# Kernel tuning notes

Hardware: AMD Instinct MI355X
Metric: run time of the kernel (lower is better)

Reference implementation:

```python
import jax, jax.numpy as jnp
import numpy as np

EMB = 1024
HEADS = 16
HEAD_DIM = EMB // HEADS
CTX = 2048
BATCH = 4
LN_EPS = 1e-5


def layer_norm(x, g, b):
    mu = jnp.mean(x, axis=-1, keepdims=True)
    var = jnp.mean(jnp.square(x - mu), axis=-1, keepdims=True)
    return (x - mu) * jax.lax.rsqrt(var + LN_EPS) * g + b


def setup_inputs() -> dict:
    key = jax.random.key(0)
    ks = jax.random.split(key, 12)
    s_in = 1.0 / np.sqrt(EMB)
    s_ff = 1.0 / np.sqrt(4 * EMB)
    return {
        "x": jax.random.normal(ks[0], (BATCH, CTX, EMB), jnp.float32),
        # per-head Q/K/V projections, no bias (matches Head linears)
        "wq": jax.random.normal(ks[1], (HEADS, EMB, HEAD_DIM), jnp.float32) * s_in,
        "wk": jax.random.normal(ks[2], (HEADS, EMB, HEAD_DIM), jnp.float32) * s_in,
        "wv": jax.random.normal(ks[3], (HEADS, EMB, HEAD_DIM), jnp.float32) * s_in,
        "w_proj": jax.random.normal(ks[4], (EMB, EMB), jnp.float32) * s_in,
        "b_proj": jnp.zeros((EMB,), jnp.float32),
        "w1": jax.random.normal(ks[5], (EMB, 4 * EMB), jnp.float32) * s_in,
        "b1": jnp.zeros((4 * EMB,), jnp.float32),
        "w2": jax.random.normal(ks[6], (4 * EMB, EMB), jnp.float32) * s_ff,
        "b2": jnp.zeros((EMB,), jnp.float32),
        "ln1_g": jnp.ones((EMB,), jnp.float32),
        "ln1_b": jnp.zeros((EMB,), jnp.float32),
        "ln2_g": jnp.ones((EMB,), jnp.float32),
        "ln2_b": jnp.zeros((EMB,), jnp.float32),
    }


def reference(x, wq, wk, wv, w_proj, b_proj, w1, b1, w2, b2, ln1_g, ln1_b, ln2_g, ln2_b):
    B, T, C = x.shape
    # --- attention branch (pre-LN) ---
    h = layer_norm(x, ln1_g, ln1_b)
    q = jnp.einsum('btc,hcd->bhtd', h, wq)
    k = jnp.einsum('btc,hcd->bhtd', h, wk)
    v = jnp.einsum('btc,hcd->bhtd', h, wv)
    scale = 1.0 / np.sqrt(HEAD_DIM)
    scores = jnp.einsum('bhtd,bhsd->bhts', q, k) * scale  # [B,H,T,T]
    causal = jnp.tril(jnp.ones((T, T), dtype=bool))
    scores = jnp.where(causal, scores, -jnp.inf)
    attn = jax.nn.softmax(scores, axis=-1)
    out = jnp.einsum('bhts,bhsd->bhtd', attn, v)
    out = out.transpose(0, 2, 1, 3).reshape(B, T, C)  # concat heads
    out = out @ w_proj.T + b_proj if False else jnp.einsum('btc,cd->btd', out, w_proj) + b_proj
    x = x + out
    # --- FFN branch (pre-LN) ---
    h2 = layer_norm(x, ln2_g, ln2_b)
    ff = jax.nn.relu(jnp.einsum('btc,cf->btf', h2, w1) + b1)
    ff = jnp.einsum('btf,fc->btc', ff, w2) + b2
    return x + ff
```

## Files before the change

kernel.cpp:

```cpp
#include <hip/hip_runtime.h>


#define DEVI __device__ __forceinline__

typedef float  f32x4  __attribute__((ext_vector_type(4)));
typedef float  f32x16 __attribute__((ext_vector_type(16)));
typedef __bf16 bf16x8 __attribute__((ext_vector_type(8)));
typedef short  s16x8  __attribute__((ext_vector_type(8)));
typedef unsigned int u32x4 __attribute__((ext_vector_type(4)));
typedef unsigned short u16;

DEVI u16 f2bf(float f) {
    return __builtin_bit_cast(u16, (__bf16)f);
}

DEVI float bf2f(u16 u) {
    unsigned v = (unsigned)u << 16;
    return __builtin_bit_cast(float, v);
}

DEVI unsigned pk2(float lo, float hi2) {
    return (unsigned)f2bf(lo) | ((unsigned)f2bf(hi2) << 16);
}

DEVI void gload_lds16(const void* g, void* l) {
    __builtin_amdgcn_global_load_lds(
        (__attribute__((address_space(1))) void*)(g),
        (__attribute__((address_space(3))) void*)(l), 16, 0, 0);
}

DEVI f32x4 mfma16(s16x8 a, s16x8 b, f32x4 c) {
    return __builtin_amdgcn_mfma_f32_16x16x32_bf16(
        __builtin_bit_cast(bf16x8, a), __builtin_bit_cast(bf16x8, b), c, 0, 0, 0);
}

DEVI f32x16 mfma32(s16x8 a, s16x8 b, f32x16 c) {
    return __builtin_amdgcn_mfma_f32_32x32x16_bf16(
        __builtin_bit_cast(bf16x8, a), __builtin_bit_cast(bf16x8, b), c, 0, 0, 0);
}

__global__ __launch_bounds__(256) void transpose_cvt(
    const float* __restrict__ src, u16* __restrict__ dst,
    int K, int N, long srcStride, long dstStride)
{
    __shared__ float t[64][65];
    src += (long)blockIdx.z * srcStride;
    dst += (long)blockIdx.z * dstStride;
    int k0 = blockIdx.x * 64, n0 = blockIdx.y * 64;
    int tx = threadIdx.x & 63, ty = threadIdx.x >> 6;
#pragma unroll
    for (int i = 0; i < 16; ++i) {
        int r = ty * 16 + i;
        t[r][tx] = src[(long)(k0 + r) * N + n0 + tx];
    }
    __syncthreads();
#pragma unroll
    for (int i = 0; i < 16; ++i) {
        int r = ty * 16 + i;
        dst[(long)(n0 + r) * K + k0 + tx] = f2bf(t[tx][r]);
    }
}

__global__ __launch_bounds__(256) void ln_bf16(
    const float* __restrict__ x, const float* __restrict__ g,
    const float* __restrict__ b, u16* __restrict__ out)
{
    int row = blockIdx.x, tid = threadIdx.x;
    const float4 v = ((const float4*)(x + (long)row * 1024))[tid];
    float s = v.x + v.y + v.z + v.w;
    float q = v.x * v.x + v.y * v.y + v.z * v.z + v.w * v.w;
#pragma unroll
    for (int m = 1; m < 64; m <<= 1) { s += __shfl_xor(s, m); q += __shfl_xor(q, m); }
    __shared__ float red[8];
    int lane = tid & 63, w = tid >> 6;
    if (lane == 0) { red[w] = s; red[w + 4] = q; }
    __syncthreads();
    s = red[0] + red[1] + red[2] + red[3];
    q = red[4] + red[5] + red[6] + red[7];
    float mu  = s * (1.0f / 1024.0f);
    float var = q * (1.0f / 1024.0f) - mu * mu;
    float rs  = rsqrtf(var + 1e-5f);
    float4 gv = ((const float4*)g)[tid];
    float4 bv = ((const float4*)b)[tid];
    ushort4 o;
    o.x = f2bf((v.x - mu) * rs * gv.x + bv.x);
    o.y = f2bf((v.y - mu) * rs * gv.y + bv.y);
    o.z = f2bf((v.z - mu) * rs * gv.z + bv.z);
    o.w = f2bf((v.w - mu) * rs * gv.w + bv.w);
    ((ushort4*)(out + (long)row * 1024))[tid] = o;
}

template <int EPI>
__global__ __launch_bounds__(512, 4) void gemm_big(
    const u16* __restrict__ A, const u16* __restrict__ Bt,
    int M, int N, int K,
    u16* __restrict__ outB, const float* __restrict__ bias,
    u16* __restrict__ qd, u16* __restrict__ kd, u16* __restrict__ vd)
{
    __shared__ alignas(16) u16 As[256 * 32];
    __shared__ alignas(16) u16 Bs[128 * 32];
    int tid = threadIdx.x;
    int lane = tid & 63, w = tid >> 6;
    int wm = w >> 1, wn = w & 1;
    int l15 = lane & 15, l4 = lane >> 4;
    long m0 = (long)blockIdx.x * 256, n0 = (long)blockIdx.y * 128;
    const u16* Ag = A + m0 * K;
    const u16* Bg = Bt + n0 * K;
    int srow_l = lane >> 2;
    int schunk = ((lane & 3) ^ (srow_l & 3)) * 8;
    int rchunk = (l4 ^ (l15 & 3)) * 8;

    f32x4 acc[4][4] = {};

    for (int kt = 0; kt < K; kt += 32) {
        gload_lds16(Ag + (long)(w * 32 + srow_l) * K + kt + schunk,
                    &As[(w * 32) * 32]);
        gload_lds16(Ag + (long)(w * 32 + 16 + srow_l) * K + kt + schunk,
                    &As[(w * 32 + 16) * 32]);
        gload_lds16(Bg + (long)(w * 16 + srow_l) * K + kt + schunk,
                    &Bs[(w * 16) * 32]);
        __syncthreads();
        s16x8 a[4], b[4];
#pragma unroll
        for (int m = 0; m < 4; ++m)
            a[m] = *(const s16x8*)&As[(wm * 64 + m * 16 + l15) * 32 + rchunk];
#pragma unroll
        for (int n = 0; n < 4; ++n)
            b[n] = *(const s16x8*)&Bs[(wn * 64 + n * 16 + l15) * 32 + rchunk];
#pragma unroll
        for (int m = 0; m < 4; ++m)
#pragma unroll
            for (int n = 0; n < 4; ++n)
                acc[m][n] = mfma16(a[m], b[n], acc[m][n]);
        __syncthreads();
    }

    long mbase = m0 + wm * 64;
    long nbase = n0 + wn * 64;
#pragma unroll
    for (int m = 0; m < 4; ++m)
#pragma unroll
        for (int n = 0; n < 4; ++n)
#pragma unroll
            for (int r = 0; r < 4; ++r) {
                long row = mbase + m * 16 + l4 * 4 + r;
                long col = nbase + n * 16 + l15;
                float val = acc[m][n][r];
                if constexpr (EPI == 0) {
                    int c = (int)col;
                    int which = c >> 10, hh = (c >> 6) & 15, dd = c & 63;
                    int bb = (int)(row >> 11), tt = (int)(row & 2047);
                    if (which == 2) {
                        vd[((long)(bb * 16 + hh) * 64 + dd) * 2048 + tt] = f2bf(val);
                    } else {
                        u16* dst = which == 0 ? qd : kd;
                        dst[((long)(bb * 16 + hh) * 2048 + tt) * 64 + dd] = f2bf(val);
                    }
                } else {
                    float t2 = val + bias[col];
                    outB[row * N + col] = f2bf(t2 > 0.f ? t2 : 0.f);
                }
            }
}

template <int EPI>
__global__ __launch_bounds__(256, 3) void gemm_bt(
    const u16* __restrict__ A, const u16* __restrict__ Bt,
    int M, int N, int K,
    float* __restrict__ outF, u16* __restrict__ outB,
    const float* __restrict__ bias, const float* __restrict__ resid,
    u16* __restrict__ qd, u16* __restrict__ kd, u16* __restrict__ vd)
{
    __shared__ alignas(16) u16 As[128 * 32];
    __shared__ alignas(16) u16 Bs[128 * 32];
    int tid = threadIdx.x;
    int lane = tid & 63, w = tid >> 6;
    int wm = w & 1, wn = w >> 1;
    int l15 = lane & 15, l4 = lane >> 4;
    long m0 = (long)blockIdx.x * 128, n0 = (long)blockIdx.y * 128;
    const u16* Ag = A + m0 * K;
    const u16* Bg = Bt + n0 * K;
    int scol = ((lane & 3) ^ ((lane >> 2) & 3)) * 8;
    int srow0 = (w * 2 + 0) * 16 + (lane >> 2);
    int srow1 = (w * 2 + 1) * 16 + (lane >> 2);
    int rchunk = (l4 ^ (l15 & 3)) * 8;

    f32x4 acc[4][4] = {};

    for (int kt = 0; kt < K; kt += 32) {
        gload_lds16(Ag + (long)srow0 * K + kt + scol, &As[(w * 2 + 0) * 512]);
        gload_lds16(Ag + (long)srow1 * K + kt + scol, &As[(w * 2 + 1) * 512]);
        gload_lds16(Bg + (long)srow0 * K + kt + scol, &Bs[(w * 2 + 0) * 512]);
        gload_lds16(Bg + (long)srow1 * K + kt + scol, &Bs[(w * 2 + 1) * 512]);
        __syncthreads();
        s16x8 a[4], b[4];
#pragma unroll
        for (int m = 0; m < 4; ++m)
            a[m] = *(const s16x8*)&As[(wm * 64 + m * 16 + l15) * 32 + rchunk];
#pragma unroll
        for (int n = 0; n < 4; ++n)
            b[n] = *(const s16x8*)&Bs[(wn * 64 + n * 16 + l15) * 32 + rchunk];
#pragma unroll
        for (int m = 0; m < 4; ++m)
#pragma unroll
            for (int n = 0; n < 4; ++n)
                acc[m][n] = mfma16(a[m], b[n], acc[m][n]);
        __syncthreads();
    }

    long mbase = m0 + wm * 64;
    long nbase = n0 + wn * 64;
#pragma unroll
    for (int m = 0; m < 4; ++m)
#pragma unroll
        for (int n = 0; n < 4; ++n)
#pragma unroll
            for (int r = 0; r < 4; ++r) {
                long row = mbase + m * 16 + l4 * 4 + r;
                long col = nbase + n * 16 + l15;
                float val = acc[m][n][r];
                if constexpr (EPI == 1) {
                    outF[row * N + col] = val + bias[col] + resid[row * N + col];
                }
            }
}

__global__ __launch_bounds__(256, 4) void attn_split(
    const u16* __restrict__ Q, const u16* __restrict__ K,
    const u16* __restrict__ Vt,
    u16* __restrict__ Op0, u16* __restrict__ Op1, float* __restrict__ ML)
{
    constexpr int PAD = 72;
    constexpr float SC2 = 0.125f * 1.44269504088896f;
    constexpr float THR = 11.5416f;
    __shared__ alignas(16) u16 Ks[2][64 * PAD];
    __shared__ alignas(16) u16 Vts[2][64 * PAD];
    __shared__ alignas(16) float xbuf[4][32];
    int tid = threadIdx.x, lane = tid & 63, w = tid >> 6;
    int l31 = lane & 31, hi = lane >> 5;
    bool h = (hi != 0);
    int p = blockIdx.x, hh = blockIdx.y, bb = blockIdx.z;
    const long hbase = ((long)(bb * 16 + hh)) * 2048 * 64;
    const long rb = ((long)(bb * 16 + hh)) * 2048;

    int srow[2], scol8[2];
#pragma unroll
    for (int i = 0; i < 2; ++i) {
        int c = tid + 256 * i;
        srow[i] = c >> 3;
        scol8[i] = (c & 7) * 8;
    }

#pragma unroll 1
    for (int ph = 0; ph < 2; ++ph) {
        int qt  = ph == 0 ? p : 15 - p;
        int kt0 = ph == 0 ? 0 : (qt + 1);
        int kt1 = qt + 1 + ph * (qt + 1);
        int ntl = kt1 - kt0;
        int q0w = qt * 128 + w * 32;
        int qv = q0w + l31;

        s16x8 bq[4];
#pragma unroll
        for (int c = 0; c < 4; ++c)
            bq[c] = *(const s16x8*)&Q[hbase + (long)(q0w + l31) * 64 + c * 16 + hi * 8];

        f32x16 o0 = {}, o1 = {};
        float mrow = -1e30f, lrow = 0.f;

        s16x8 kr[2], vr[2];
        {
            const u16* Kg = K + hbase + (long)kt0 * 64 * 64;
            const u16* Vg = Vt + hbase + (long)kt0 * 64;
#pragma unroll
            for (int i = 0; i < 2; ++i) {
                s16x8 k0 = *(const s16x8*)&Kg[srow[i] * 64 + scol8[i]];
                s16x8 v0 = *(const s16x8*)&Vg[(long)srow[i] * 2048 + scol8[i]];
                *(s16x8*)&Ks[0][srow[i] * PAD + scol8[i]]  = k0;
                *(s16x8*)&Vts[0][srow[i] * PAD + scol8[i]] = v0;
            }
            if (ntl > 1) {
                const u16* Kg1 = K + hbase + (long)(kt0 + 1) * 64 * 64;
                const u16* Vg1 = Vt + hbase + (long)(kt0 + 1) * 64;
#pragma unroll
                for (int i = 0; i < 2; ++i) {
                    kr[i] = *(const s16x8*)&Kg1[srow[i] * 64 + scol8[i]];
                    vr[i] = *(const s16x8*)&Vg1[(long)srow[i] * 2048 + scol8[i]];
                }
            }
        }
        __syncthreads();

#pragma unroll 1
        for (int j = 0; j < ntl; ++j) {
            int kt = kt0 + j;
            int cur = j & 1;
            if (j + 1 < ntl) {
#pragma unroll
                for (int i = 0; i < 2; ++i) {
                    *(s16x8*)&Ks[cur ^ 1][srow[i] * PAD + scol8[i]]  = kr[i];
                    *(s16x8*)&Vts[cur ^ 1][srow[i] * PAD + scol8[i]] = vr[i];
                }
            }
            if (j + 2 < ntl) {
                const u16* Kg = K + hbase + (long)(kt + 2) * 64 * 64;
                const u16* Vg = Vt + hbase + (long)(kt + 2) * 64;
#pragma unroll
                for (int i = 0; i < 2; ++i) {
                    kr[i] = *(const s16x8*)&Kg[srow[i] * 64 + scol8[i]];
                    vr[i] = *(const s16x8*)&Vg[(long)srow[i] * 2048 + scol8[i]];
                }
            }

#pragma unroll
            for (int k2 = 0; k2 < 2; ++k2) {
                int kbase = kt * 64 + k2 * 32;
                if (kbase <= q0w + 31) {
                    f32x16 s = {};
                    __builtin_amdgcn_s_setprio(1);
#pragma unroll
                    for (int c = 0; c < 4; ++c) {
                        s16x8 ak = *(const s16x8*)&Ks[cur][(k2 * 32 + l31) * PAD + c * 16 + hi * 8];
                        s = mfma32(ak, bq[c], s);
                    }
                    __builtin_amdgcn_s_setprio(0);

                    if (kbase + 31 > q0w) {
                        int d = qv - (kbase + 4 * hi);
#pragma unroll
                        for (int r = 0; r < 16; ++r) {
                            int pat = (r & 3) + 8 * (r >> 2);
                            if (pat > d) s[r] = -3.0e38f;
                        }
                    }

                    float t8[8], t4[4];
#pragma unroll
                    for (int r = 0; r < 8; ++r) t8[r] = fmaxf(s[r], s[r + 8]);
#pragma unroll
                    for (int r = 0; r < 4; ++r) t4[r] = fmaxf(t8[r], t8[r + 4]);
                    float pm = fmaxf(fmaxf(t4[0], t4[2]), fmaxf(t4[1], t4[3]));
                    pm *= SC2;
                    pm = fmaxf(pm, __shfl_xor(pm, 32));

                    int allok = __all(pm - mrow <= THR);
                    float ef = 1.f;
                    if (!allok) {
                        float mn = fmaxf(mrow, pm);
                        ef = exp2f(mrow - mn);
                        mrow = mn;
                    }
#pragma unroll
                    for (int r = 0; r < 16; ++r) s[r] = exp2f(fmaf(s[r], SC2, -mrow));
                    float a8[8], a4[4];
#pragma unroll
                    for (int r = 0; r < 8; ++r) a8[r] = s[r] + s[r + 8];
#pragma unroll
                    for (int r = 0; r < 4; ++r) a4[r] = a8[r] + a8[r + 4];
                    float rsum = (a4[0] + a4[1]) + (a4[2] + a4[3]);
                    rsum += __shfl_xor(rsum, 32);

                    if (!allok) {
                        lrow = lrow * ef + rsum;
                        xbuf[w][l31] = ef;
#pragma unroll
                        for (int rr = 0; rr < 4; ++rr) {
                            f32x4 efv = *(const f32x4*)&xbuf[w][rr * 8 + hi * 4];
#pragma unroll
                            for (int j2 = 0; j2 < 4; ++j2) {
                                o0[rr * 4 + j2] *= efv[j2];
                                o1[rr * 4 + j2] *= efv[j2];
                            }
                        }
                    } else {
                        lrow += rsum;
                    }

                    unsigned c0 = pk2(s[0],  s[1]),  c1 = pk2(s[2],  s[3]);
                    unsigned c2 = pk2(s[4],  s[5]),  c3 = pk2(s[6],  s[7]);
                    unsigned c4 = pk2(s[8],  s[9]),  c5 = pk2(s[10], s[11]);
                    unsigned c6 = pk2(s[12], s[13]), c7 = pk2(s[14], s[15]);
                    unsigned x0 = __shfl_xor((int)c0, 32), x1 = __shfl_xor((int)c1, 32);
                    unsigned x2 = __shfl_xor((int)c2, 32), x3 = __shfl_xor((int)c3, 32);
                    unsigned x4 = __shfl_xor((int)c4, 32), x5 = __shfl_xor((int)c5, 32);
                    unsigned x6 = __shfl_xor((int)c6, 32), x7 = __shfl_xor((int)c7, 32);
                    u32x4 w0 = { h ? x2 : c0, h ? x3 : c1, h ? c2 : x0, h ? c3 : x1 };
                    u32x4 w1 = { h ? x6 : c4, h ? x7 : c5, h ? c6 : x4, h ? c7 : x5 };
                    s16x8 pa0 = __builtin_bit_cast(s16x8, w0);
                    s16x8 pa1 = __builtin_bit_cast(s16x8, w1);

                    __builtin_amdgcn_s_setprio(1);
#pragma unroll
                    for (int ks = 0; ks < 2; ++ks) {
                        s16x8 pa = ks ? pa1 : pa0;
                        s16x8 bv0 = *(const s16x8*)&Vts[cur][(l31) * PAD + k2 * 32 + ks * 16 + hi * 8];
                        s16x8 bv1 = *(const s16x8*)&Vts[cur][(32 + l31) * PAD + k2 * 32 + ks * 16 + hi * 8];
                        o0 = mfma32(pa, bv0, o0);
                        o1 = mfma32(pa, bv1, o1);
                    }
                    __builtin_amdgcn_s_setprio(0);
                }
            }
            __syncthreads();
        }

        u16* Ops = ph ? Op1 : Op0;
#pragma unroll
        for (int r = 0; r < 16; ++r) {
            int t = q0w + ((r & 3) + 8 * (r >> 2)) + 4 * hi;
            long ro = (rb + t) * 64;
            Ops[ro + l31]      = f2bf(o0[r]);
            Ops[ro + 32 + l31] = f2bf(o1[r]);
        }
        if (hi == 0) {
            long mrow_i = rb + q0w + l31;
            ML[ph * 262144 + mrow_i]          = mrow;
            ML[ph * 262144 + 131072 + mrow_i] = lrow;
        }
        __syncthreads();
    }
}

__global__ __launch_bounds__(256) void attn_combine(
    const u16* __restrict__ Op0, const u16* __restrict__ Op1,
    const float* __restrict__ ML, u16* __restrict__ O)
{
    int tid = threadIdx.x;
    long row = (long)blockIdx.x * 16 + (tid >> 4);
    int d0 = (tid & 15) * 4;
    float m1 = ML[row],          l1 = ML[131072 + row];
    float m2 = ML[262144 + row], l2 = ML[393216 + row];
    float mm = fmaxf(m1, m2);
    float w1 = exp2f(m1 - mm), w2 = exp2f(m2 - mm);
    float inv = 1.0f / (w1 * l1 + w2 * l2);
    ushort4 a = *(const ushort4*)&Op0[row * 64 + d0];
    ushort4 b = *(const ushort4*)&Op1[row * 64 + d0];
    ushort4 o;
    o.x = f2bf((w1 * bf2f(a.x) + w2 * bf2f(b.x)) * inv);
    o.y = f2bf((w1 * bf2f(a.y) + w2 * bf2f(b.y)) * inv);
    o.z = f2bf((w1 * bf2f(a.z) + w2 * bf2f(b.z)) * inv);
    o.w = f2bf((w1 * bf2f(a.w) + w2 * bf2f(b.w)) * inv);
    int bb = (int)(row >> 15), hh2 = (int)((row >> 11) & 15), t = (int)(row & 2047);
    *(ushort4*)&O[((long)(bb * 2048 + t)) * 1024 + hh2 * 64 + d0] = o;
}

extern "C" void kernel_launch(void* const* d_in, const int* in_sizes, int n_in,
                              void* d_out, int out_size, void* d_ws, size_t ws_size,
                              hipStream_t stream)
{
    const float* x      = (const float*)d_in[0];
    const float* wq     = (const float*)d_in[1];
    const float* wk     = (const float*)d_in[2];
    const float* wv     = (const float*)d_in[3];
    const float* w_proj = (const float*)d_in[4];
    const float* b_proj = (const float*)d_in[5];
    const float* w1     = (const float*)d_in[6];
    const float* b1     = (const float*)d_in[7];
    const float* w2     = (const float*)d_in[8];
    const float* b2     = (const float*)d_in[9];
    const float* ln1_g  = (const float*)d_in[10];
    const float* ln1_b  = (const float*)d_in[11];
    const float* ln2_g  = (const float*)d_in[12];
    const float* ln2_b  = (const float*)d_in[13];

    char* ws = (char*)d_ws;
    u16*   WQKVt = (u16*)(ws + 0);
    u16*   WPt   = (u16*)(ws + 6291456);
    u16*   W1t   = (u16*)(ws + 8388608);
    u16*   W2t   = (u16*)(ws + 16777216);
    u16*   H     = (u16*)(ws + 25165824);
    float* ML    = (float*)(ws + 25165824);
    u16*   Qb    = (u16*)(ws + 41943040);
    u16*   Kb    = (u16*)(ws + 58720256);
    u16*   Vb    = (u16*)(ws + 75497472);
    u16*   Ob    = (u16*)(ws + 92274688);
    u16*   FF    = (u16*)(ws + 41943040);
    float* X1    = (float*)(ws + 109051904);
    u16*   Op0   = (u16*)(ws + 109051904);
    u16*   Op1   = (u16*)(ws + 109051904 + 16777216);
    float* out   = (float*)d_out;

    transpose_cvt<<<dim3(16, 1, 16), 256, 0, stream>>>(wq, WQKVt,           1024, 64, 65536, 65536);
    transpose_cvt<<<dim3(16, 1, 16), 256, 0, stream>>>(wk, WQKVt + 1048576, 1024, 64, 65536, 65536);
    transpose_cvt<<<dim3(16, 1, 16), 256, 0, stream>>>(wv, WQKVt + 2097152, 1024, 64, 65536, 65536);
    transpose_cvt<<<dim3(16, 16, 1), 256, 0, stream>>>(w_proj, WPt, 1024, 1024, 0, 0);
    transpose_cvt<<<dim3(16, 64, 1), 256, 0, stream>>>(w1, W1t, 1024, 4096, 0, 0);
    transpose_cvt<<<dim3(64, 16, 1), 256, 0, stream>>>(w2, W2t, 4096, 1024, 0, 0);

    ln_bf16<<<8192, 256, 0, stream>>>(x, ln1_g, ln1_b, H);

    gemm_big<0><<<dim3(32, 24), 512, 0, stream>>>(H, WQKVt, 8192, 3072, 1024,
        nullptr, nullptr, Qb, Kb, Vb);

    attn_split<<<dim3(16, 16, 4), 256, 0, stream>>>(Qb, Kb, Vb, Op0, Op1, ML);
    attn_combine<<<8192, 256, 0, stream>>>(Op0, Op1, ML, Ob);

    gemm_bt<1><<<dim3(64, 8), 256, 0, stream>>>(Ob, WPt, 8192, 1024, 1024,
        X1, nullptr, b_proj, x, nullptr, nullptr, nullptr);

    ln_bf16<<<8192, 256, 0, stream>>>(X1, ln2_g, ln2_b, H);

    gemm_big<2><<<dim3(32, 32), 512, 0, stream>>>(H, W1t, 8192, 4096, 1024,
        FF, b1, nullptr, nullptr, nullptr);

    gemm_bt<1><<<dim3(64, 8), 256, 0, stream>>>(FF, W2t, 8192, 1024, 4096,
        out, nullptr, b2, X1, nullptr, nullptr, nullptr);
}
```

Baseline: 411.1 us.

## Process full 64-key tile per online-softmax step instead of two 32-key halves

Merges the two 32-key sub-iterations of the attention inner loop into one step over 64 keys. Both QK^T score blocks are computed first, then a single max/rescale/exp/sum pass runs over both. This halves the per-tile row-max reductions, cross-lane shuffles, wave votes and accumulator rescales. In exchange it holds two 16-float score vectors live at once, which raises register pressure. When the second half is fully masked it still runs exp and PV MFMAs on -inf values, where before it skipped them.

```diff
diff --git a/kernel.cpp b/kernel.cpp
--- a/kernel.cpp
+++ b/kernel.cpp
@@ -312,94 +312,129 @@
                 }
             }
 
-#pragma unroll
-            for (int k2 = 0; k2 < 2; ++k2) {
-                int kbase = kt * 64 + k2 * 32;
-                if (kbase <= q0w + 31) {
-                    f32x16 s = {};
+            int kb0 = kt * 64;
+            if (kb0 <= q0w + 31) {
+                bool live1 = (kb0 + 32 <= q0w + 31);
+
+                f32x16 s0 = {}, s1;
+                __builtin_amdgcn_s_setprio(1);
+#pragma unroll
+                for (int c = 0; c < 4; ++c) {
+                    s16x8 ak = *(const s16x8*)&Ks[cur][(l31) * PAD + c * 16 + hi * 8];
+                    s0 = mfma32(ak, bq[c], s0);
+                }
+                __builtin_amdgcn_s_setprio(0);
+                if (live1) {
+                    f32x16 z = {};
                     __builtin_amdgcn_s_setprio(1);
 #pragma unroll
                     for (int c = 0; c < 4; ++c) {
-                        s16x8 ak = *(const s16x8*)&Ks[cur][(k2 * 32 + l31) * PAD + c * 16 + hi * 8];
-                        s = mfma32(ak, bq[c], s);
+                        s16x8 ak = *(const s16x8*)&Ks[cur][(32 + l31) * PAD + c * 16 + hi * 8];
+                        z = mfma32(ak, bq[c], z);
                     }
                     __builtin_amdgcn_s_setprio(0);
-
-                    if (kbase + 31 > q0w) {
-                        int d = qv - (kbase + 4 * hi);
-#pragma unroll
-                        for (int r = 0; r < 16; ++r) {
-                            int pat = (r & 3) + 8 * (r >> 2);
-                            if (pat > d) s[r] = -3.0e38f;
+                    s1 = z;
+                } else {
+#pragma unroll
+                    for (int r = 0; r < 16; ++r) s1[r] = -3.0e38f;
+                }
+
+                if (kb0 + 31 > q0w) {
+                    int d = qv - (kb0 + 4 * hi);
+#pragma unroll
+                    for (int r = 0; r < 16; ++r) {
+                        int pat = (r & 3) + 8 * (r >> 2);
+                        if (pat > d) s0[r] = -3.0e38f;
+                    }
+                }
+                if (live1 && kb0 + 63 > q0w) {
+                    int d = qv - (kb0 + 32 + 4 * hi);
+#pragma unroll
+                    for (int r = 0; r < 16; ++r) {
+                        int pat = (r & 3) + 8 * (r >> 2);
+                        if (pat > d) s1[r] = -3.0e38f;
+                    }
+                }
+
+                float m16[16];
+#pragma unroll
+                for (int r = 0; r < 16; ++r) m16[r] = fmaxf(s0[r], s1[r]);
+                float m8[8], m4[4];
+#pragma unroll
+                for (int r = 0; r < 8; ++r) m8[r] = fmaxf(m16[r], m16[r + 8]);
+#pragma unroll
+                for (int r = 0; r < 4; ++r) m4[r] = fmaxf(m8[r], m8[r + 4]);
+                float pm = fmaxf(fmaxf(m4[0], m4[1]), fmaxf(m4[2], m4[3]));
+                pm *= SC2;
+                pm = fmaxf(pm, __shfl_xor(pm, 32));
+
+                int allok = __all(pm - mrow <= THR);
+                float ef = 1.f;
+                if (!allok) {
+                    float mn = fmaxf(mrow, pm);
+                    ef = exp2f(mrow - mn);
+                    mrow = mn;
+                }
+#pragma unroll
+                for (int r = 0; r < 16; ++r) s0[r] = exp2f(fmaf(s0[r], SC2, -mrow));
+#pragma unroll
+                for (int r = 0; r < 16; ++r) s1[r] = exp2f(fmaf(s1[r], SC2, -mrow));
+                float a16[16];
+#pragma unroll
+                for (int r = 0; r < 16; ++r) a16[r] = s0[r] + s1[r];
+                float a8[8], a4[4];
+#pragma unroll
+                for (int r = 0; r < 8; ++r) a8[r] = a16[r] + a16[r + 8];
+#pragma unroll
+                for (int r = 0; r < 4; ++r) a4[r] = a8[r] + a8[r + 4];
+                float rsum = (a4[0] + a4[1]) + (a4[2] + a4[3]);
+                rsum += __shfl_xor(rsum, 32);
+
+                if (!allok) {
+                    lrow = lrow * ef + rsum;
+                    xbuf[w][l31] = ef;
+#pragma unroll
+                    for (int rr = 0; rr < 4; ++rr) {
+                        f32x4 efv = *(const f32x4*)&xbuf[w][rr * 8 + hi * 4];
+#pragma unroll
+                        for (int j2 = 0; j2 < 4; ++j2) {
+                            o0[rr * 4 + j2] *= efv[j2];
+                            o1[rr * 4 + j2] *= efv[j2];
                         }
                     }
-
-                    float t8[8], t4[4];
-#pragma unroll
-                    for (int r = 0; r < 8; ++r) t8[r] = fmaxf(s[r], s[r + 8]);
-#pragma unroll
-                    for (int r = 0; r < 4; ++r) t4[r] = fmaxf(t8[r], t8[r + 4]);
-                    float pm = fmaxf(fmaxf(t4[0], t4[2]), fmaxf(t4[1], t4[3]));
-                    pm *= SC2;
-                    pm = fmaxf(pm, __shfl_xor(pm, 32));
-
-                    int allok = __all(pm - mrow <= THR);
-                    float ef = 1.f;
-                    if (!allok) {
-                        float mn = fmaxf(mrow, pm);
-                        ef = exp2f(mrow - mn);
-                        mrow = mn;
-                    }
-#pragma unroll
-                    for (int r = 0; r < 16; ++r) s[r] = exp2f(fmaf(s[r], SC2, -mrow));
-                    float a8[8], a4[4];
-#pragma unroll
-                    for (int r = 0; r < 8; ++r) a8[r] = s[r] + s[r + 8];
-#pragma unroll
-                    for (int r = 0; r < 4; ++r) a4[r] = a8[r] + a8[r + 4];
-                    float rsum = (a4[0] + a4[1]) + (a4[2] + a4[3]);
-                    rsum += __shfl_xor(rsum, 32);
-
-                    if (!allok) {
-                        lrow = lrow * ef + rsum;
-                        xbuf[w][l31] = ef;
-#pragma unroll
-                        for (int rr = 0; rr < 4; ++rr) {
-                            f32x4 efv = *(const f32x4*)&xbuf[w][rr * 8 + hi * 4];
-#pragma unroll
-                            for (int j2 = 0; j2 < 4; ++j2) {
-                                o0[rr * 4 + j2] *= efv[j2];
-                                o1[rr * 4 + j2] *= efv[j2];
-                            }
-                        }
-                    } else {
-                        lrow += rsum;
-                    }
-
-                    unsigned c0 = pk2(s[0],  s[1]),  c1 = pk2(s[2],  s[3]);
-                    unsigned c2 = pk2(s[4],  s[5]),  c3 = pk2(s[6],  s[7]);
-                    unsigned c4 = pk2(s[8],  s[9]),  c5 = pk2(s[10], s[11]);
-                    unsigned c6 = pk2(s[12], s[13]), c7 = pk2(s[14], s[15]);
+                } else {
+                    lrow += rsum;
+                }
+
+                s16x8 pa[2][2];
+#pragma unroll
+                for (int sub = 0; sub < 2; ++sub) {
+                    const f32x16& sv = sub ? s1 : s0;
+                    unsigned c0 = pk2(sv[0],  sv[1]),  c1 = pk2(sv[2],  sv[3]);
+                    unsigned c2 = pk2(sv[4],  sv[5]),  c3 = pk2(sv[6],  sv[7]);
+                    unsigned c4 = pk2(sv[8],  sv[9]),  c5 = pk2(sv[10], sv[11]);
+                    unsigned c6 = pk2(sv[12], sv[13]), c7 = pk2(sv[14], sv[15]);
                     unsigned x0 = __shfl_xor((int)c0, 32), x1 = __shfl_xor((int)c1, 32);
                     unsigned x2 = __shfl_xor((int)c2, 32), x3 = __shfl_xor((int)c3, 32);
                     unsigned x4 = __shfl_xor((int)c4, 32), x5 = __shfl_xor((int)c5, 32);
                     unsigned x6 = __shfl_xor((int)c6, 32), x7 = __shfl_xor((int)c7, 32);
                     u32x4 w0 = { h ? x2 : c0, h ? x3 : c1, h ? c2 : x0, h ? c3 : x1 };
                     u32x4 w1 = { h ? x6 : c4, h ? x7 : c5, h ? c6 : x4, h ? c7 : x5 };
-                    s16x8 pa0 = __builtin_bit_cast(s16x8, w0);
-                    s16x8 pa1 = __builtin_bit_cast(s16x8, w1);
-
-                    __builtin_amdgcn_s_setprio(1);
+                    pa[sub][0] = __builtin_bit_cast(s16x8, w0);
+                    pa[sub][1] = __builtin_bit_cast(s16x8, w1);
+                }
+
+                __builtin_amdgcn_s_setprio(1);
+#pragma unroll
+                for (int sub = 0; sub < 2; ++sub)
 #pragma unroll
                     for (int ks = 0; ks < 2; ++ks) {
-                        s16x8 pa = ks ? pa1 : pa0;
-                        s16x8 bv0 = *(const s16x8*)&Vts[cur][(l31) * PAD + k2 * 32 + ks * 16 + hi * 8];
-                        s16x8 bv1 = *(const s16x8*)&Vts[cur][(32 + l31) * PAD + k2 * 32 + ks * 16 + hi * 8];
-                        o0 = mfma32(pa, bv0, o0);
-                        o1 = mfma32(pa, bv1, o1);
+                        s16x8 bv0 = *(const s16x8*)&Vts[cur][(l31) * PAD + sub * 32 + ks * 16 + hi * 8];
+                        s16x8 bv1 = *(const s16x8*)&Vts[cur][(32 + l31) * PAD + sub * 32 + ks * 16 + hi * 8];
+                        o0 = mfma32(pa[sub][ks], bv0, o0);
+                        o1 = mfma32(pa[sub][ks], bv1, o1);
                     }
-                    __builtin_amdgcn_s_setprio(0);
-                }
+                __builtin_amdgcn_s_setprio(0);
             }
             __syncthreads();
         }
```

Result: slower. 436.4 us (+6.1%).
